# Kernel tuning notes

Hardware: AMD Instinct MI355X
Metric: run time of the kernel (lower is better)

Reference implementation:

```python
import jax, jax.numpy as jnp
import numpy as np


def setup_inputs() -> dict:
    key = jax.random.key(0)
    k1, k2 = jax.random.split(key)
    B, C, F = 1024, 500, 512
    x = jax.random.normal(k1, (B, F), dtype=jnp.float32)
    means = jax.random.normal(k2, (C, F), dtype=jnp.float32)
    variance = jnp.ones((1,), dtype=jnp.float32)
    return {"x": x, "means": means, "variance": variance}


def reference(x, means, variance):
    # non-deep_nno eval path: std = self.variance parameter
    xs = x / variance  # [B, F] / [1] broadcast
    # pairwise L2 distances: [B, C]
    diff = xs[:, None, :] - means[None, :, :]  # [B, C, F]
    cumulative_diff = jnp.sqrt(jnp.sum(diff * diff, axis=-1))  # [B, C]
    exponent = -cumulative_diff
    probs = jax.nn.softmax(exponent, axis=1)
    return (probs, exponent, cumulative_diff)
```

## Files before the change

kernel.cpp:

```cpp
#include <hip/hip_runtime.h>
#include <hip/hip_bf16.h>
#include <math.h>

#define NB 1024
#define NC 500
#define NCP 512
#define NF 512
#define LSTR 520

typedef __attribute__((ext_vector_type(8))) short bf16x8;
typedef __attribute__((ext_vector_type(4))) float f32x4;

union bfpack { bf16x8 v; __hip_bfloat162 h[4]; };

__global__ __launch_bounds__(512) void ncm_dist_fused(
    const float* __restrict__ x, const float* __restrict__ means,
    const float* __restrict__ variance, float* __restrict__ out)
{
    __shared__ ushort sA[32][LSTR];
    __shared__ ushort sB[64][LSTR];
    __shared__ float  sNx[32];
    __shared__ float  sNm[64];

    const int t    = threadIdx.x;
    const int w    = t >> 6;
    const int lane = t & 63;
    const int fr   = lane & 15;
    const int g    = lane >> 4;
    const int b0   = blockIdx.x * 32;
    const int c0   = blockIdx.y * 64;
    const float inv_var = 1.0f / variance[0];

    #pragma unroll
    for (int j = 0; j < 12; ++j) {
        const int ri = w * 12 + j;
        const float* src;
        ushort* dst;
        float* nrm;
        float scale;
        bool zero = false;
        if (ri < 32) {
            src = x + (size_t)(b0 + ri) * NF;  dst = &sA[ri][0];
            nrm = &sNx[ri];                    scale = inv_var;
        } else {
            const int cm = c0 + ri - 32;
            src = means + (size_t)cm * NF;     dst = &sB[ri - 32][0];
            nrm = &sNm[ri - 32];               scale = 1.0f;
            zero = (cm >= NC);
        }

        float4 v0, v1;
        if (!zero) {
            v0 = *reinterpret_cast<const float4*>(&src[lane * 8]);
            v1 = *reinterpret_cast<const float4*>(&src[lane * 8 + 4]);
            v0.x *= scale; v0.y *= scale; v0.z *= scale; v0.w *= scale;
            v1.x *= scale; v1.y *= scale; v1.z *= scale; v1.w *= scale;
        } else {
            v0 = make_float4(0.f, 0.f, 0.f, 0.f);
            v1 = v0;
        }
        bfpack p;
        p.h[0] = __float22bfloat162_rn(make_float2(v0.x, v0.y));
        p.h[1] = __float22bfloat162_rn(make_float2(v0.z, v0.w));
        p.h[2] = __float22bfloat162_rn(make_float2(v1.x, v1.y));
        p.h[3] = __float22bfloat162_rn(make_float2(v1.z, v1.w));
        *reinterpret_cast<bf16x8*>(&dst[lane * 8]) = p.v;

        float s = v0.x * v0.x + v0.y * v0.y + v0.z * v0.z + v0.w * v0.w
                + v1.x * v1.x + v1.y * v1.y + v1.z * v1.z + v1.w * v1.w;
        #pragma unroll
        for (int off = 32; off > 0; off >>= 1) s += __shfl_xor(s, off, 64);
        if (lane == 0) *nrm = s;
    }
    __syncthreads();

    const int ar = (w >> 2) * 16 + fr;
    const int br = (w & 3) * 16 + fr;
    const ushort* ap = &sA[ar][g * 8];
    const ushort* bp = &sB[br][g * 8];

    f32x4 acc = {0.f, 0.f, 0.f, 0.f};
    #pragma unroll
    for (int ks = 0; ks < 16; ++ks) {
        bf16x8 a = *reinterpret_cast<const bf16x8*>(ap + ks * 32);
        bf16x8 b = *reinterpret_cast<const bf16x8*>(bp + ks * 32);
        acc = __builtin_amdgcn_mfma_f32_16x16x32_bf16(a, b, acc, 0, 0, 0);
    }

    const int c = c0 + (w & 3) * 16 + fr;
    if (c < NC) {
        const float nmc = sNm[(w & 3) * 16 + fr];
        float* expo  = out + (size_t)NB * NC;
        float* cdiff = out + (size_t)2 * NB * NC;
        #pragma unroll
        for (int r = 0; r < 4; ++r) {
            const int bl = (w >> 2) * 16 + g * 4 + r;
            const int b  = b0 + bl;
            float d2 = sNx[bl] + nmc - 2.0f * acc[r];
            float d = sqrtf(fmaxf(d2, 0.0f));
            expo[(size_t)b * NC + c]  = -d;
            cdiff[(size_t)b * NC + c] = d;
        }
    }
}

__global__ __launch_bounds__(64) void ncm_softmax_kernel(float* __restrict__ out)
{
    const int b = blockIdx.x;
    const int lane = threadIdx.x;
    const float* expo = out + (size_t)NB * NC + (size_t)b * NC;
    float* probs = out + (size_t)b * NC;

    const int base = lane * 8;
    const bool val0 = base + 3 < NC;
    const bool val1 = base + 7 < NC;
    const float4 ninf = make_float4(-1e30f, -1e30f, -1e30f, -1e30f);

    float4 v0 = val0 ? *reinterpret_cast<const float4*>(&expo[base])     : ninf;
    float4 v1 = val1 ? *reinterpret_cast<const float4*>(&expo[base + 4]) : ninf;

    float m = fmaxf(fmaxf(fmaxf(v0.x, v0.y), fmaxf(v0.z, v0.w)),
                    fmaxf(fmaxf(v1.x, v1.y), fmaxf(v1.z, v1.w)));
    #pragma unroll
    for (int off = 32; off > 0; off >>= 1)
        m = fmaxf(m, __shfl_xor(m, off, 64));

    float4 e0, e1;
    e0.x = expf(v0.x - m); e0.y = expf(v0.y - m);
    e0.z = expf(v0.z - m); e0.w = expf(v0.w - m);
    e1.x = expf(v1.x - m); e1.y = expf(v1.y - m);
    e1.z = expf(v1.z - m); e1.w = expf(v1.w - m);

    float s = e0.x + e0.y + e0.z + e0.w + e1.x + e1.y + e1.z + e1.w;
    #pragma unroll
    for (int off = 32; off > 0; off >>= 1)
        s += __shfl_xor(s, off, 64);
    float inv = 1.0f / s;

    e0.x *= inv; e0.y *= inv; e0.z *= inv; e0.w *= inv;
    e1.x *= inv; e1.y *= inv; e1.z *= inv; e1.w *= inv;

    if (val0) *reinterpret_cast<float4*>(&probs[base])     = e0;
    if (val1) *reinterpret_cast<float4*>(&probs[base + 4]) = e1;
}

extern "C" void kernel_launch(void* const* d_in, const int* in_sizes, int n_in,
                              void* d_out, int out_size, void* d_ws, size_t ws_size,
                              hipStream_t stream) {
    const float* x        = (const float*)d_in[0];
    const float* means    = (const float*)d_in[1];
    const float* variance = (const float*)d_in[2];
    float* out = (float*)d_out;

    dim3 g(NB / 32, NCP / 64);
    ncm_dist_fused<<<g, 512, 0, stream>>>(x, means, variance, out);
    ncm_softmax_kernel<<<NB, 64, 0, stream>>>(out);
}
```

Baseline: 17.74 us.

## Fuse softmax into distance kernel via last-block atomic counter per row tile

Each distance block increments a per-row-tile atomic counter after writing its exponent tile. The last of the 8 column blocks for that tile then computes the row softmax for its 32 rows directly, so the separate softmax kernel launch goes away. A memset of the counters is added to the stream. Correctness depends on acquire/release visibility of the other blocks' writes. When no workspace is available, the code falls back to the old two-kernel path.

```diff
diff --git a/kernel.cpp b/kernel.cpp
--- a/kernel.cpp
+++ b/kernel.cpp
@@ -15,12 +15,14 @@
 
 __global__ __launch_bounds__(512) void ncm_dist_fused(
     const float* __restrict__ x, const float* __restrict__ means,
-    const float* __restrict__ variance, float* __restrict__ out)
+    const float* __restrict__ variance, float* __restrict__ out,
+    uint* __restrict__ cnt)
 {
     __shared__ ushort sA[32][LSTR];
     __shared__ ushort sB[64][LSTR];
     __shared__ float  sNx[32];
     __shared__ float  sNm[64];
+    __shared__ uint   s_old;
 
     const int t    = threadIdx.x;
     const int w    = t >> 6;
@@ -88,10 +90,10 @@
     }
 
     const int c = c0 + (w & 3) * 16 + fr;
+    float* expo  = out + (size_t)NB * NC;
+    float* cdiff = out + (size_t)2 * NB * NC;
     if (c < NC) {
         const float nmc = sNm[(w & 3) * 16 + fr];
-        float* expo  = out + (size_t)NB * NC;
-        float* cdiff = out + (size_t)2 * NB * NC;
         #pragma unroll
         for (int r = 0; r < 4; ++r) {
             const int bl = (w >> 2) * 16 + g * 4 + r;
@@ -102,6 +104,55 @@
             cdiff[(size_t)b * NC + c] = d;
         }
     }
+
+    __syncthreads();
+    if (t == 0) {
+        s_old = __hip_atomic_fetch_add(&cnt[blockIdx.x], 1u,
+                                       __ATOMIC_ACQ_REL,
+                                       __HIP_MEMORY_SCOPE_AGENT);
+    }
+    __syncthreads();
+    if (s_old != 7u) return;
+
+    float* probs = out;
+    #pragma unroll
+    for (int i = 0; i < 4; ++i) {
+        const int b = b0 + w * 4 + i;
+        const float* erow = expo + (size_t)b * NC;
+        float* prow = probs + (size_t)b * NC;
+
+        const int base = lane * 8;
+        const bool val0 = base + 3 < NC;
+        const bool val1 = base + 7 < NC;
+        const float4 ninf = make_float4(-1e30f, -1e30f, -1e30f, -1e30f);
+
+        float4 v0 = val0 ? *reinterpret_cast<const float4*>(&erow[base])     : ninf;
+        float4 v1 = val1 ? *reinterpret_cast<const float4*>(&erow[base + 4]) : ninf;
+
+        float m = fmaxf(fmaxf(fmaxf(v0.x, v0.y), fmaxf(v0.z, v0.w)),
+                        fmaxf(fmaxf(v1.x, v1.y), fmaxf(v1.z, v1.w)));
+        #pragma unroll
+        for (int off = 32; off > 0; off >>= 1)
+            m = fmaxf(m, __shfl_xor(m, off, 64));
+
+        float4 e0, e1;
+        e0.x = expf(v0.x - m); e0.y = expf(v0.y - m);
+        e0.z = expf(v0.z - m); e0.w = expf(v0.w - m);
+        e1.x = expf(v1.x - m); e1.y = expf(v1.y - m);
+        e1.z = expf(v1.z - m); e1.w = expf(v1.w - m);
+
+        float s = e0.x + e0.y + e0.z + e0.w + e1.x + e1.y + e1.z + e1.w;
+        #pragma unroll
+        for (int off = 32; off > 0; off >>= 1)
+            s += __shfl_xor(s, off, 64);
+        const float inv = 1.0f / s;
+
+        e0.x *= inv; e0.y *= inv; e0.z *= inv; e0.w *= inv;
+        e1.x *= inv; e1.y *= inv; e1.z *= inv; e1.w *= inv;
+
+        if (val0) *reinterpret_cast<float4*>(&prow[base])     = e0;
+        if (val1) *reinterpret_cast<float4*>(&prow[base + 4]) = e1;
+    }
 }
 
 __global__ __launch_bounds__(64) void ncm_softmax_kernel(float* __restrict__ out)
@@ -142,6 +193,96 @@
 
     if (val0) *reinterpret_cast<float4*>(&probs[base])     = e0;
     if (val1) *reinterpret_cast<float4*>(&probs[base + 4]) = e1;
+}
+
+__global__ __launch_bounds__(512) void ncm_dist_only(
+    const float* __restrict__ x, const float* __restrict__ means,
+    const float* __restrict__ variance, float* __restrict__ out)
+{
+    __shared__ ushort sA[32][LSTR];
+    __shared__ ushort sB[64][LSTR];
+    __shared__ float  sNx[32];
+    __shared__ float  sNm[64];
+
+    const int t    = threadIdx.x;
+    const int w    = t >> 6;
+    const int lane = t & 63;
+    const int fr   = lane & 15;
+    const int g    = lane >> 4;
+    const int b0   = blockIdx.x * 32;
+    const int c0   = blockIdx.y * 64;
+    const float inv_var = 1.0f / variance[0];
+
+    #pragma unroll
+    for (int j = 0; j < 12; ++j) {
+        const int ri = w * 12 + j;
+        const float* src;
+        ushort* dst;
+        float* nrm;
+        float scale;
+        bool zero = false;
+        if (ri < 32) {
+            src = x + (size_t)(b0 + ri) * NF;  dst = &sA[ri][0];
+            nrm = &sNx[ri];                    scale = inv_var;
+        } else {
+            const int cm = c0 + ri - 32;
+            src = means + (size_t)cm * NF;     dst = &sB[ri - 32][0];
+            nrm = &sNm[ri - 32];               scale = 1.0f;
+            zero = (cm >= NC);
+        }
+        float4 v0, v1;
+        if (!zero) {
+            v0 = *reinterpret_cast<const float4*>(&src[lane * 8]);
+            v1 = *reinterpret_cast<const float4*>(&src[lane * 8 + 4]);
+            v0.x *= scale; v0.y *= scale; v0.z *= scale; v0.w *= scale;
+            v1.x *= scale; v1.y *= scale; v1.z *= scale; v1.w *= scale;
+        } else {
+            v0 = make_float4(0.f, 0.f, 0.f, 0.f);
+            v1 = v0;
+        }
+        bfpack p;
+        p.h[0] = __float22bfloat162_rn(make_float2(v0.x, v0.y));
+        p.h[1] = __float22bfloat162_rn(make_float2(v0.z, v0.w));
+        p.h[2] = __float22bfloat162_rn(make_float2(v1.x, v1.y));
+        p.h[3] = __float22bfloat162_rn(make_float2(v1.z, v1.w));
+        *reinterpret_cast<bf16x8*>(&dst[lane * 8]) = p.v;
+
+        float s = v0.x * v0.x + v0.y * v0.y + v0.z * v0.z + v0.w * v0.w
+                + v1.x * v1.x + v1.y * v1.y + v1.z * v1.z + v1.w * v1.w;
+        #pragma unroll
+        for (int off = 32; off > 0; off >>= 1) s += __shfl_xor(s, off, 64);
+        if (lane == 0) *nrm = s;
+    }
+    __syncthreads();
+
+    const int ar = (w >> 2) * 16 + fr;
+    const int br = (w & 3) * 16 + fr;
+    const ushort* ap = &sA[ar][g * 8];
+    const ushort* bp = &sB[br][g * 8];
+
+    f32x4 acc = {0.f, 0.f, 0.f, 0.f};
+    #pragma unroll
+    for (int ks = 0; ks < 16; ++ks) {
+        bf16x8 a = *reinterpret_cast<const bf16x8*>(ap + ks * 32);
+        bf16x8 b = *reinterpret_cast<const bf16x8*>(bp + ks * 32);
+        acc = __builtin_amdgcn_mfma_f32_16x16x32_bf16(a, b, acc, 0, 0, 0);
+    }
+
+    const int c = c0 + (w & 3) * 16 + fr;
+    if (c < NC) {
+        const float nmc = sNm[(w & 3) * 16 + fr];
+        float* expo  = out + (size_t)NB * NC;
+        float* cdiff = out + (size_t)2 * NB * NC;
+        #pragma unroll
+        for (int r = 0; r < 4; ++r) {
+            const int bl = (w >> 2) * 16 + g * 4 + r;
+            const int b  = b0 + bl;
+            float d2 = sNx[bl] + nmc - 2.0f * acc[r];
+            float d = sqrtf(fmaxf(d2, 0.0f));
+            expo[(size_t)b * NC + c]  = -d;
+            cdiff[(size_t)b * NC + c] = d;
+        }
+    }
 }
 
 extern "C" void kernel_launch(void* const* d_in, const int* in_sizes, int n_in,
@@ -153,6 +294,14 @@
     float* out = (float*)d_out;
 
     dim3 g(NB / 32, NCP / 64);
-    ncm_dist_fused<<<g, 512, 0, stream>>>(x, means, variance, out);
+
+    if (ws_size >= 32 * sizeof(uint)) {
+        uint* cnt = (uint*)d_ws;
+        hipMemsetAsync(cnt, 0, 32 * sizeof(uint), stream);
+        ncm_dist_fused<<<g, 512, 0, stream>>>(x, means, variance, out, cnt);
+        return;
+    }
+
+    ncm_dist_only<<<g, 512, 0, stream>>>(x, means, variance, out);
     ncm_softmax_kernel<<<NB, 64, 0, stream>>>(out);
 }
```

After: 36.04 us. 2.03x slower.
